# Kernel tuning notes

Hardware: AMD Instinct MI355X
Metric: run time of the kernel (lower is better)

The kernel has to match this reference:

```python
import jax, jax.numpy as jnp
import numpy as np

D = 1024  # embed_dim

def setup_inputs() -> dict:
    key = jax.random.key(0)
    ks = jax.random.split(key, 5)
    s = 1.0 / np.sqrt(D)  # keep weight magnitudes sane
    x = jax.random.normal(ks[0], (2, 4096, D), dtype=jnp.float32)
    Wq = jax.random.normal(ks[1], (D, D), dtype=jnp.float32) * s
    Wk = jax.random.normal(ks[2], (D, D), dtype=jnp.float32) * s
    Wv = jax.random.normal(ks[3], (D, D), dtype=jnp.float32) * s
    Wo = jax.random.normal(ks[4], (D, D), dtype=jnp.float32) * s
    return {"x": x, "Wq": Wq, "Wk": Wk, "Wv": Wv, "Wo": Wo}

def reference(x, Wq, Wk, Wv, Wo):
    # torch nn.Linear(no bias): y = x @ W.T
    q = jnp.einsum('bsd,ed->bse', x, Wq)
    k = jnp.einsum('bsd,ed->bse', x, Wk)
    v = jnp.einsum('bsd,ed->bse', x, Wv)
    embed_dim = x.shape[-1]
    scores = jnp.einsum('bqd,bkd->bqk', q, k) / jnp.sqrt(jnp.asarray(embed_dim, x.dtype))
    attn = jax.nn.softmax(scores, axis=-1)  # dropout is identity in eval mode (p=0)
    out = jnp.einsum('bqk,bkd->bqd', attn, v)
    out = jnp.einsum('bsd,ed->bse', out, Wo)
    return out
```

## Files before the change

kernel.cpp:

```cpp
#include <hip/hip_runtime.h>
#include <hip/hip_bf16.h>

using short8 = __attribute__((ext_vector_type(8))) short;
using f32x4  = __attribute__((ext_vector_type(4))) float;

__device__ __forceinline__ unsigned short f2bf(float f) {
  union { float f; unsigned int u; } x; x.f = f;
  unsigned int r = (x.u + 0x7fffu + ((x.u >> 16) & 1u)) >> 16;
  return (unsigned short)r;
}

__device__ __forceinline__ void gld_lds16(const short* gp, short* lp) {
  __builtin_amdgcn_global_load_lds((const __attribute__((address_space(1))) void*)gp,
                                   (__attribute__((address_space(3))) void*)lp, 16, 0, 0);
}

__global__ __launch_bounds__(256) void cast_all(const float4* __restrict__ x,
                                                const float4* __restrict__ Wq,
                                                const float4* __restrict__ Wk,
                                                const float4* __restrict__ Wv,
                                                const float4* __restrict__ Wo,
                                                short* __restrict__ xb,
                                                short* __restrict__ wqkv,
                                                short* __restrict__ wo) {
  const int i = blockIdx.x * 256 + threadIdx.x;
  const float4* src;
  short* dst;
  if (i < 2097152) {
    src = x + i;
    dst = xb + 4ll * i;
  } else {
    const int j = i - 2097152;
    const int w = j >> 18;
    const int off = j & 262143;
    src = (w == 0 ? Wq : w == 1 ? Wk : w == 2 ? Wv : Wo) + off;
    dst = (w < 3 ? wqkv + (long long)w * 1048576 : wo) + 4ll * off;
  }
  float4 f = *src;
  short4 o;
  o.x = (short)f2bf(f.x); o.y = (short)f2bf(f.y);
  o.z = (short)f2bf(f.z); o.w = (short)f2bf(f.w);
  *(short4*)dst = o;
}

__global__ __launch_bounds__(256) void zero_f32(float* __restrict__ p, int n) {
  int i = blockIdx.x * 256 + threadIdx.x;
  if (i < n) p[i] = 0.f;
}

template <int MODE>
__global__ __launch_bounds__(256) void gemm_bt(const short* __restrict__ A,
                                               const short* __restrict__ B,
                                               void* __restrict__ Cv,
                                               float* __restrict__ sums,
                                               int K, int ldc, float scale,
                                               long long aStr, long long bStr,
                                               long long cStr, int gy, int ng) {
  __shared__ short lA[128 * 64];
  __shared__ short lB[128 * 64];
  const int bid = blockIdx.x;
  const int bx  = bid / ng;
  const int g   = bid % ng;
  const int by  = g % gy;
  const long long z = g / gy;
  const int tid = threadIdx.x;
  const int w   = tid >> 6;
  const int l   = tid & 63;
  const int wm  = w >> 1, wn = w & 1;
  const long long tm = (long long)by * 128;
  const long long tn = (long long)bx * 128;
  A += z * aStr;
  B += z * bStr;

  const bool swp = (MODE == 2) ? (bx < 16) : true;

  f32x4 acc[4][4] = {};

  const int lr   = l >> 3;
  const int scw  = ((l & 7) ^ (lr & 7)) * 8;
  const int q4   = l >> 4;
  const int fr   = l & 15;
  const int xr   = fr & 7;

  for (int k0 = 0; k0 < K; k0 += 64) {
#pragma unroll
    for (int t = 0; t < 4; ++t) {
      const int seg = w * 4 + t;
      gld_lds16(A + (tm + seg * 8 + lr) * (long long)K + k0 + scw, &lA[seg * 512]);
      gld_lds16(B + (tn + seg * 8 + lr) * (long long)K + k0 + scw, &lB[seg * 512]);
    }
    __syncthreads();
#pragma unroll
    for (int kk = 0; kk < 64; kk += 32) {
      const int cs = ((((kk >> 3)) + q4) ^ xr) << 3;
      short8 af[4], bfr[4];
#pragma unroll
      for (int i = 0; i < 4; ++i)
        af[i] = *(const short8*)&lA[(wm * 64 + i * 16 + fr) * 64 + cs];
#pragma unroll
      for (int j = 0; j < 4; ++j)
        bfr[j] = *(const short8*)&lB[(wn * 64 + j * 16 + fr) * 64 + cs];
      if (swp) {
#pragma unroll
        for (int i = 0; i < 4; ++i)
#pragma unroll
          for (int j = 0; j < 4; ++j)
            acc[i][j] = __builtin_amdgcn_mfma_f32_16x16x32_bf16(bfr[j], af[i], acc[i][j], 0, 0, 0);
      } else {
#pragma unroll
        for (int i = 0; i < 4; ++i)
#pragma unroll
          for (int j = 0; j < 4; ++j)
            acc[i][j] = __builtin_amdgcn_mfma_f32_16x16x32_bf16(af[i], bfr[j], acc[i][j], 0, 0, 0);
      }
    }
    __syncthreads();
  }

  const int rb = (l >> 4) * 4;

  if (MODE == 0) {
    float* dst = (float*)Cv + z * cStr;
#pragma unroll
    for (int i = 0; i < 4; ++i) {
      const long long row = tm + wm * 64 + i * 16 + fr;
#pragma unroll
      for (int j = 0; j < 4; ++j) {
        const long long colb = tn + wn * 64 + j * 16 + rb;
        *(f32x4*)((float*)dst + row * ldc + colb) = acc[i][j];
      }
    }
  } else if (MODE == 2) {
    const int cb0 = (int)(tn & 1023) + wn * 64;
    if (swp) {
      const int region = (int)(tn >> 10);
      unsigned short* dst = (unsigned short*)Cv + (long long)region * 8388608ll;
#pragma unroll
      for (int i = 0; i < 4; ++i) {
        const long long row = tm + wm * 64 + i * 16 + fr;
#pragma unroll
        for (int j = 0; j < 4; ++j) {
          const int colb = cb0 + j * 16 + rb;
          short4 pk;
          pk.x = (short)f2bf(acc[i][j][0]); pk.y = (short)f2bf(acc[i][j][1]);
          pk.z = (short)f2bf(acc[i][j][2]); pk.w = (short)f2bf(acc[i][j][3]);
          *(short4*)(dst + row * 1024 + colb) = pk;
        }
      }
    } else {
      unsigned short* dst = (unsigned short*)Cv + 16777216ll;
#pragma unroll
      for (int i = 0; i < 4; ++i)
#pragma unroll
        for (int j = 0; j < 4; ++j) {
          const long long row0 = tm + wm * 64 + i * 16 + rb;
          const long long b = row0 >> 12, s0 = row0 & 4095;
          const int c = cb0 + j * 16 + fr;
          short4 pk;
          pk.x = (short)f2bf(acc[i][j][0]); pk.y = (short)f2bf(acc[i][j][1]);
          pk.z = (short)f2bf(acc[i][j][2]); pk.w = (short)f2bf(acc[i][j][3]);
          *(short4*)(dst + b * 4194304ll + (long long)c * 4096 + s0) = pk;
        }
    }
  } else if (MODE == 4) {
    unsigned short* dst = (unsigned short*)Cv + z * cStr;
    float* sm = sums + z * 4096;
#pragma unroll
    for (int i = 0; i < 4; ++i) {
      const long long row = tm + wm * 64 + i * 16 + fr;
      float rs = 0.f;
#pragma unroll
      for (int j = 0; j < 4; ++j) {
        const long long colb = tn + wn * 64 + j * 16 + rb;
        short4 pk;
        float e0 = __expf(acc[i][j][0] * scale);
        float e1 = __expf(acc[i][j][1] * scale);
        float e2 = __expf(acc[i][j][2] * scale);
        float e3 = __expf(acc[i][j][3] * scale);
        rs += (e0 + e1) + (e2 + e3);
        pk.x = (short)f2bf(e0); pk.y = (short)f2bf(e1);
        pk.z = (short)f2bf(e2); pk.w = (short)f2bf(e3);
        *(short4*)(dst + row * ldc + colb) = pk;
      }
      rs += __shfl_xor(rs, 16);
      rs += __shfl_xor(rs, 32);
      if (l < 16) atomicAdd(sm + tm + wm * 64 + i * 16 + l, rs);
    }
  } else {
    unsigned short* dst = (unsigned short*)Cv + z * cStr;
    const float* sm = sums + z * 4096;
#pragma unroll
    for (int i = 0; i < 4; ++i) {
      const long long row = tm + wm * 64 + i * 16 + fr;
      const float inv = 1.0f / sm[row];
#pragma unroll
      for (int j = 0; j < 4; ++j) {
        const long long colb = tn + wn * 64 + j * 16 + rb;
        short4 pk;
        pk.x = (short)f2bf(acc[i][j][0] * inv); pk.y = (short)f2bf(acc[i][j][1] * inv);
        pk.z = (short)f2bf(acc[i][j][2] * inv); pk.w = (short)f2bf(acc[i][j][3] * inv);
        *(short4*)(dst + row * ldc + colb) = pk;
      }
    }
  }
}

extern "C" void kernel_launch(void* const* d_in, const int* in_sizes, int n_in,
                              void* d_out, int out_size, void* d_ws, size_t ws_size,
                              hipStream_t stream) {
  const float* x  = (const float*)d_in[0];
  const float* Wq = (const float*)d_in[1];
  const float* Wk = (const float*)d_in[2];
  const float* Wv = (const float*)d_in[3];
  const float* Wo = (const float*)d_in[4];
  float* out = (float*)d_out;

  char* ws = (char*)d_ws;
  short* xb   = (short*)ws;
  short* wqkv = (short*)(ws + (16ll << 20));
  short* wo   = wqkv + 3145728;
  short* q    = (short*)(ws + (24ll << 20));
  short* k    = q + 8388608;
  short* vt   = q + 16777216;
  short* ao   = (short*)(ws + (72ll << 20));
  short* sc   = (short*)(ws + (88ll << 20));
  float* sums = (float*)ws;

  const bool batched = ws_size >= 159383552ull;
  dim3 blk(256);

  cast_all<<<12288, blk, 0, stream>>>((const float4*)x, (const float4*)Wq,
                                      (const float4*)Wk, (const float4*)Wv,
                                      (const float4*)Wo, xb, wqkv, wo);

  gemm_bt<2><<<24 * 64, blk, 0, stream>>>(xb, wqkv, q, nullptr, 1024, 1024, 1.f,
                                          0, 0, 0, 64, 64);

  if (batched) {
    zero_f32<<<32, blk, 0, stream>>>(sums, 8192);
    gemm_bt<4><<<32 * 64, blk, 0, stream>>>(q, k, sc, sums, 1024, 4096, 0.03125f,
                                            4194304ll, 4194304ll, 16777216ll, 32, 64);
    gemm_bt<5><<<8 * 64, blk, 0, stream>>>(sc, vt, ao, sums, 4096, 1024, 1.f,
                                           16777216ll, 4194304ll, 4194304ll, 32, 64);
  } else {
    for (int b = 0; b < 2; ++b) {
      short* qb  = q  + (long long)b * 4194304;
      short* kb  = k  + (long long)b * 4194304;
      short* vb  = vt + (long long)b * 4194304;
      short* aob = ao + (long long)b * 4194304;
      zero_f32<<<16, blk, 0, stream>>>(sums, 4096);
      gemm_bt<4><<<32 * 32, blk, 0, stream>>>(qb, kb, sc, sums, 1024, 4096, 0.03125f,
                                              0, 0, 0, 32, 32);
      gemm_bt<5><<<8 * 32, blk, 0, stream>>>(sc, vb, aob, sums, 4096, 1024, 1.f,
                                             0, 0, 0, 32, 32);
    }
  }

  gemm_bt<0><<<8 * 64, blk, 0, stream>>>(ao, wo, out, nullptr, 1024, 1024, 1.f,
                                         0, 0, 0, 64, 64);
}
```

Before: 349.8 us.

## Fold output projection into value weights via precomputed Wo·Wv

Precomputes the combined weight Wo·Wv as a small 1024x1024 GEMM, and uses it in place of Wv in the QKV projection. The attention output can then be written directly as the final fp32 result, so the separate output-projection GEMM and the intermediate bf16 attention-output buffer are removed. The Wv transpose and the zeroing of the row-sum buffer are merged into the cast kernel, which drops a separate zero launch. This trades a 2*4096x1024x1024 GEMM for one 1024^3 GEMM plus a transpose, and adds a second bf16 rounding on the fused weights, which may affect accuracy.

```diff
diff --git a/kernel.cpp b/kernel.cpp
--- a/kernel.cpp
+++ b/kernel.cpp
@@ -15,37 +15,62 @@
                                    (__attribute__((address_space(3))) void*)lp, 16, 0, 0);
 }
 
-__global__ __launch_bounds__(256) void cast_all(const float4* __restrict__ x,
-                                                const float4* __restrict__ Wq,
-                                                const float4* __restrict__ Wk,
-                                                const float4* __restrict__ Wv,
-                                                const float4* __restrict__ Wo,
+__global__ __launch_bounds__(256) void cast_all(const float* __restrict__ x,
+                                                const float* __restrict__ Wq,
+                                                const float* __restrict__ Wk,
+                                                const float* __restrict__ Wv,
+                                                const float* __restrict__ Wo,
                                                 short* __restrict__ xb,
                                                 short* __restrict__ wqkv,
-                                                short* __restrict__ wo) {
-  const int i = blockIdx.x * 256 + threadIdx.x;
-  const float4* src;
-  short* dst;
-  if (i < 2097152) {
-    src = x + i;
-    dst = xb + 4ll * i;
+                                                short* __restrict__ wo,
+                                                short* __restrict__ wvT,
+                                                float4* __restrict__ sums4) {
+  const int bid = blockIdx.x;
+  const int tid = threadIdx.x;
+  if (bid < 11264) {
+    const float4* src;
+    short* dst;
+    const int i = bid * 256 + tid;
+    if (bid < 8192) {
+      src = (const float4*)x + i;
+      dst = xb + 4ll * i;
+    } else {
+      const int j = i - 2097152;
+      const int w = j >> 18;
+      const int off = j & 262143;
+      src = (const float4*)(w == 0 ? Wq : w == 1 ? Wk : Wo) + off;
+      dst = (w == 0 ? wqkv : w == 1 ? wqkv + 1048576 : wo) + 4ll * off;
+    }
+    float4 f = *src;
+    short4 o;
+    o.x = (short)f2bf(f.x); o.y = (short)f2bf(f.y);
+    o.z = (short)f2bf(f.z); o.w = (short)f2bf(f.w);
+    *(short4*)dst = o;
+    if (bid < 8) sums4[bid * 256 + tid] = float4{0.f, 0.f, 0.f, 0.f};
   } else {
-    const int j = i - 2097152;
-    const int w = j >> 18;
-    const int off = j & 262143;
-    src = (w == 0 ? Wq : w == 1 ? Wk : w == 2 ? Wv : Wo) + off;
-    dst = (w < 3 ? wqkv + (long long)w * 1048576 : wo) + 4ll * off;
-  }
-  float4 f = *src;
-  short4 o;
-  o.x = (short)f2bf(f.x); o.y = (short)f2bf(f.y);
-  o.z = (short)f2bf(f.z); o.w = (short)f2bf(f.w);
-  *(short4*)dst = o;
-}
-
-__global__ __launch_bounds__(256) void zero_f32(float* __restrict__ p, int n) {
-  int i = blockIdx.x * 256 + threadIdx.x;
-  if (i < n) p[i] = 0.f;
+    __shared__ short tls[64][65];
+    const int t  = bid - 11264;
+    const int bx = t & 15, by = t >> 4;
+    const int r  = tid >> 4;
+    const int c4 = (tid & 15) * 4;
+#pragma unroll
+    for (int s = 0; s < 4; ++s) {
+      float4 f = *(const float4*)(Wv + (long long)(by * 64 + r + s * 16) * 1024 + bx * 64 + c4);
+      tls[r + s * 16][c4 + 0] = (short)f2bf(f.x);
+      tls[r + s * 16][c4 + 1] = (short)f2bf(f.y);
+      tls[r + s * 16][c4 + 2] = (short)f2bf(f.z);
+      tls[r + s * 16][c4 + 3] = (short)f2bf(f.w);
+    }
+    __syncthreads();
+#pragma unroll
+    for (int s = 0; s < 4; ++s) {
+      const int a = r + s * 16;
+      short4 o;
+      o.x = tls[c4 + 0][a]; o.y = tls[c4 + 1][a];
+      o.z = tls[c4 + 2][a]; o.w = tls[c4 + 3][a];
+      *(short4*)(wvT + (long long)(bx * 64 + a) * 1024 + by * 64 + c4) = o;
+    }
+  }
 }
 
 template <int MODE>
@@ -119,15 +144,18 @@
 
   const int rb = (l >> 4) * 4;
 
-  if (MODE == 0) {
-    float* dst = (float*)Cv + z * cStr;
+  if (MODE == 1) {
+    unsigned short* dst = (unsigned short*)Cv + z * cStr;
 #pragma unroll
     for (int i = 0; i < 4; ++i) {
       const long long row = tm + wm * 64 + i * 16 + fr;
 #pragma unroll
       for (int j = 0; j < 4; ++j) {
         const long long colb = tn + wn * 64 + j * 16 + rb;
-        *(f32x4*)((float*)dst + row * ldc + colb) = acc[i][j];
+        short4 pk;
+        pk.x = (short)f2bf(acc[i][j][0]); pk.y = (short)f2bf(acc[i][j][1]);
+        pk.z = (short)f2bf(acc[i][j][2]); pk.w = (short)f2bf(acc[i][j][3]);
+        *(short4*)(dst + row * ldc + colb) = pk;
       }
     }
   } else if (MODE == 2) {
@@ -187,7 +215,7 @@
       if (l < 16) atomicAdd(sm + tm + wm * 64 + i * 16 + l, rs);
     }
   } else {
-    unsigned short* dst = (unsigned short*)Cv + z * cStr;
+    float* dst = (float*)Cv + z * cStr;
     const float* sm = sums + z * 4096;
 #pragma unroll
     for (int i = 0; i < 4; ++i) {
@@ -196,10 +224,10 @@
 #pragma unroll
       for (int j = 0; j < 4; ++j) {
         const long long colb = tn + wn * 64 + j * 16 + rb;
-        short4 pk;
-        pk.x = (short)f2bf(acc[i][j][0] * inv); pk.y = (short)f2bf(acc[i][j][1] * inv);
-        pk.z = (short)f2bf(acc[i][j][2] * inv); pk.w = (short)f2bf(acc[i][j][3] * inv);
-        *(short4*)(dst + row * ldc + colb) = pk;
+        f32x4 o;
+        o[0] = acc[i][j][0] * inv; o[1] = acc[i][j][1] * inv;
+        o[2] = acc[i][j][2] * inv; o[3] = acc[i][j][3] * inv;
+        *(f32x4*)(dst + row * ldc + colb) = o;
       }
     }
   }
@@ -222,40 +250,39 @@
   short* q    = (short*)(ws + (24ll << 20));
   short* k    = q + 8388608;
   short* vt   = q + 16777216;
-  short* ao   = (short*)(ws + (72ll << 20));
+  float* sums = (float*)(ws + (72ll << 20));
+  short* wvT  = (short*)(ws + (88ll << 20));
   short* sc   = (short*)(ws + (88ll << 20));
-  float* sums = (float*)ws;
+  short* wvo  = wqkv + 2097152;
 
   const bool batched = ws_size >= 159383552ull;
   dim3 blk(256);
 
-  cast_all<<<12288, blk, 0, stream>>>((const float4*)x, (const float4*)Wq,
-                                      (const float4*)Wk, (const float4*)Wv,
-                                      (const float4*)Wo, xb, wqkv, wo);
+  cast_all<<<11520, blk, 0, stream>>>(x, Wq, Wk, Wv, Wo, xb, wqkv, wo, wvT,
+                                      (float4*)sums);
+
+  gemm_bt<1><<<8 * 8, blk, 0, stream>>>(wo, wvT, wvo, nullptr, 1024, 1024, 1.f,
+                                        0, 0, 0, 8, 8);
 
   gemm_bt<2><<<24 * 64, blk, 0, stream>>>(xb, wqkv, q, nullptr, 1024, 1024, 1.f,
                                           0, 0, 0, 64, 64);
 
   if (batched) {
-    zero_f32<<<32, blk, 0, stream>>>(sums, 8192);
     gemm_bt<4><<<32 * 64, blk, 0, stream>>>(q, k, sc, sums, 1024, 4096, 0.03125f,
                                             4194304ll, 4194304ll, 16777216ll, 32, 64);
-    gemm_bt<5><<<8 * 64, blk, 0, stream>>>(sc, vt, ao, sums, 4096, 1024, 1.f,
+    gemm_bt<6><<<8 * 64, blk, 0, stream>>>(sc, vt, out, sums, 4096, 1024, 1.f,
                                            16777216ll, 4194304ll, 4194304ll, 32, 64);
   } else {
     for (int b = 0; b < 2; ++b) {
       short* qb  = q  + (long long)b * 4194304;
       short* kb  = k  + (long long)b * 4194304;
       short* vb  = vt + (long long)b * 4194304;
-      short* aob = ao + (long long)b * 4194304;
-      zero_f32<<<16, blk, 0, stream>>>(sums, 4096);
-      gemm_bt<4><<<32 * 32, blk, 0, stream>>>(qb, kb, sc, sums, 1024, 4096, 0.03125f,
+      float* ob  = out + (long long)b * 4194304;
+      float* smb = sums + (long long)b * 4096;
+      gemm_bt<4><<<32 * 32, blk, 0, stream>>>(qb, kb, sc, smb, 1024, 4096, 0.03125f,
                                               0, 0, 0, 32, 32);
-      gemm_bt<5><<<8 * 32, blk, 0, stream>>>(sc, vb, aob, sums, 4096, 1024, 1.f,
+      gemm_bt<6><<<8 * 32, blk, 0, stream>>>(sc, vb, ob, smb, 4096, 1024, 1.f,
                                              0, 0, 0, 32, 32);
     }
   }
-
-  gemm_bt<0><<<8 * 64, blk, 0, stream>>>(ao, wo, out, nullptr, 1024, 1024, 1.f,
-                                         0, 0, 0, 64, 64);
-}
+}
```

After: 348.8 us. About the same (-0.3%).
